# Kernel optimization log

Hardware: AMD Instinct MI355X
Metric: run time of the kernel (lower is better)

## Reference

```python
import jax, jax.numpy as jnp
import numpy as np

N = 50000
E = 800000
IN_C = 256
HID = 256
OUT_C = 64
HEADS = 4
NEG_SLOPE = 0.2  # PyG GATConv default leaky_relu slope


def gat_conv(x, edge_index, W, a_src, a_dst, bias, heads, concat):
    """PyG-style GATConv (add_self_loops=True, eval mode so no dropout).
    x: [N, F_in]; W: [F_in, heads*C]; a_src/a_dst: [heads, C]; bias: [heads*C] or [C].
    """
    n = x.shape[0]
    # add self loops
    loops = jnp.arange(n, dtype=edge_index.dtype)
    src = jnp.concatenate([edge_index[0], loops])
    dst = jnp.concatenate([edge_index[1], loops])
    h = (x @ W).reshape(n, heads, -1)               # [N, H, C]
    alpha_src = jnp.einsum('nhc,hc->nh', h, a_src)  # [N, H]
    alpha_dst = jnp.einsum('nhc,hc->nh', h, a_dst)
    e = jax.nn.leaky_relu(alpha_src[src] + alpha_dst[dst], NEG_SLOPE)  # [E', H]
    # segment softmax over incoming edges of each dst node
    m = jax.ops.segment_max(e, dst, num_segments=n)        # [N, H]
    w = jnp.exp(e - m[dst])
    denom = jax.ops.segment_sum(w, dst, num_segments=n)    # [N, H]
    att = w / (denom[dst] + 1e-16)                          # [E', H]
    out = jax.ops.segment_sum(h[src] * att[:, :, None], dst, num_segments=n)  # [N, H, C]
    out = out.reshape(n, -1) if concat else out.mean(axis=1)
    return out + bias


def setup_inputs() -> dict:
    key = jax.random.key(0)
    ks = jax.random.split(key, 10)
    c1 = HID // HEADS  # per-head channels of layer 1
    s_in = 1.0 / np.sqrt(IN_C)
    s_hid = 1.0 / np.sqrt(HID)
    return {
        'x': jax.random.normal(ks[0], (N, IN_C), dtype=jnp.float32),
        'edge_index': jax.random.randint(ks[1], (2, E), 0, N, dtype=jnp.int64),
        'W1': jax.random.normal(ks[2], (IN_C, HEADS * c1), dtype=jnp.float32) * s_in,
        'a_src1': jax.random.normal(ks[3], (HEADS, c1), dtype=jnp.float32) * s_in,
        'a_dst1': jax.random.normal(ks[4], (HEADS, c1), dtype=jnp.float32) * s_in,
        'b1': jnp.zeros((HEADS * c1,), dtype=jnp.float32),
        'W2': jax.random.normal(ks[5], (HID, OUT_C), dtype=jnp.float32) * s_hid,
        'a_src2': jax.random.normal(ks[6], (1, OUT_C), dtype=jnp.float32) * s_hid,
        'a_dst2': jax.random.normal(ks[7], (1, OUT_C), dtype=jnp.float32) * s_hid,
        'b2': jnp.zeros((OUT_C,), dtype=jnp.float32),
    }


def reference(x, edge_index, W1, a_src1, a_dst1, b1, W2, a_src2, a_dst2, b2):
    h = gat_conv(x, edge_index, W1, a_src1, a_dst1, b1, heads=HEADS, concat=True)
    h = jax.nn.elu(h)
    # dropout: eval mode -> identity
    return gat_conv(h, edge_index, W2, a_src2, a_dst2, b2, heads=1, concat=False)
```

## Files before the change

kernel.cpp:

```cpp
#include <hip/hip_runtime.h>
#include <math.h>

#define NN 50000
#define NE 800000
#define ET (NE + NN)
#define FIN 256
#define HIDC 256
#define OC 64
#define NH 4
#define NEG 0.2f
#define CAP 64
#define NSTRIPES (NN / 16)
#define NGROUPS ((NSTRIPES + 1) / 2)

typedef __attribute__((ext_vector_type(8))) short bf16x8;
typedef __attribute__((ext_vector_type(4))) float f32x4;

__device__ __forceinline__ unsigned short f2bf(float f) {
    unsigned u = __float_as_uint(f);
    unsigned r = (u + 0x7FFFu + ((u >> 16) & 1u)) >> 16;
    return (unsigned short)r;
}
__device__ __forceinline__ float bflo(unsigned v) { return __uint_as_float(v << 16); }
__device__ __forceinline__ float bfhi(unsigned v) { return __uint_as_float(v & 0xffff0000u); }

#define SCB 8
#define NB_SC ((ET + 256 * SCB - 1) / (256 * SCB))
#define NB_CV (NN * FIN / 8 / 256)
#define NB_P1 32
#define NB_P2 8

__device__ __forceinline__ void pack_body(const float* __restrict__ W,
                                          unsigned short* __restrict__ Bp,
                                          int N, int NTL, int t) {
    int lane = t & 63;
    int ntl = (t >> 6) % NTL;
    int ks = ((t >> 6) / NTL) & 7;
    int hy = t / (64 * NTL * 8);
    int col = hy * NTL * 16 + ntl * 16 + (lane & 15);
    int k0 = ks * 32 + (lane >> 4) * 8;
#pragma unroll
    for (int i = 0; i < 8; i++) Bp[(size_t)t * 8 + i] = f2bf(W[(k0 + i) * N + col]);
}

__global__ void k_prep(const int* __restrict__ ei, int* __restrict__ cnt,
                       unsigned short* __restrict__ esrc,
                       const float* __restrict__ x, unsigned short* __restrict__ xb,
                       const float* __restrict__ W1, unsigned short* __restrict__ Bp1,
                       const float* __restrict__ W2, unsigned short* __restrict__ Bp2) {
    int b = blockIdx.x, tid = threadIdx.x;
    if (b < NB_SC) {
        int ebase = b * (256 * SCB) + tid;
        int s[SCB], d[SCB], k[SCB];
        bool v[SCB];
#pragma unroll
        for (int i = 0; i < SCB; i++) {
            int e = ebase + i * 256;
            v[i] = (e < ET);
            s[i] = 0; d[i] = 0;
            if (v[i]) {
                if (e < NE) { s[i] = ei[e]; d[i] = ei[NE + e]; }
                else { s[i] = d[i] = e - NE; }
            }
        }
#pragma unroll
        for (int i = 0; i < SCB; i++)
            if (v[i]) k[i] = atomicAdd(&cnt[d[i]], 1);
#pragma unroll
        for (int i = 0; i < SCB; i++)
            if (v[i] && k[i] < CAP) esrc[(size_t)d[i] * CAP + k[i]] = (unsigned short)s[i];
    } else if (b < NB_SC + NB_CV) {
        int i = ((b - NB_SC) * 256 + tid) * 8;
        float4 f0 = *(const float4*)&x[i];
        float4 f1 = *(const float4*)&x[i + 4];
        uint4 o;
        o.x = (unsigned)f2bf(f0.x) | ((unsigned)f2bf(f0.y) << 16);
        o.y = (unsigned)f2bf(f0.z) | ((unsigned)f2bf(f0.w) << 16);
        o.z = (unsigned)f2bf(f1.x) | ((unsigned)f2bf(f1.y) << 16);
        o.w = (unsigned)f2bf(f1.z) | ((unsigned)f2bf(f1.w) << 16);
        *(uint4*)&xb[i] = o;
    } else if (b < NB_SC + NB_CV + NB_P1) {
        pack_body(W1, Bp1, HIDC, 8, (b - NB_SC - NB_CV) * 256 + tid);
    } else {
        pack_body(W2, Bp2, OC, 4, (b - NB_SC - NB_CV - NB_P1) * 256 + tid);
    }
}

template <int NTL, int NHEADS>
__global__ void __launch_bounds__(256) k_gemm(const unsigned short* __restrict__ A,
                                              const unsigned short* __restrict__ Bp,
                                              unsigned short* __restrict__ D, int N,
                                              const float* __restrict__ aS,
                                              const float* __restrict__ aD,
                                              float* __restrict__ asOut,
                                              float* __restrict__ adOut) {
    constexpr int TOT = 8 * NTL * 64 * 8;
    constexpr int HPH = (NTL * 16) / 64;
    const unsigned short* bsrc = Bp + (size_t)blockIdx.y * TOT;
    int wave = threadIdx.x >> 6, lane = threadIdx.x & 63;
    int l15 = lane & 15, lh = lane >> 4;
    int coloff = blockIdx.y * NTL * 16;
    float aSv[NTL], aDv[NTL];
#pragma unroll
    for (int nt = 0; nt < NTL; nt++) {
        aSv[nt] = aS[coloff + nt * 16 + l15];
        aDv[nt] = aD[coloff + nt * 16 + l15];
    }
    for (int g = blockIdx.x * 4 + wave; g < NGROUPS; g += gridDim.x * 4) {
        int st0 = g * 2;
        bool two = (st0 + 1 < NSTRIPES);
        const unsigned short* arow0 = A + (size_t)(st0 * 16 + l15) * 256 + lh * 8;
        const unsigned short* arow1 = two ? arow0 + 16 * 256 : arow0;
        bf16x8 a0[8], a1[8];
#pragma unroll
        for (int ks = 0; ks < 8; ks++) a0[ks] = *(const bf16x8*)(arow0 + ks * 32);
#pragma unroll
        for (int ks = 0; ks < 8; ks++) a1[ks] = *(const bf16x8*)(arow1 + ks * 32);
        f32x4 acc[2][NTL];
#pragma unroll
        for (int m = 0; m < 2; m++)
#pragma unroll
            for (int t = 0; t < NTL; t++) acc[m][t] = (f32x4){0.f, 0.f, 0.f, 0.f};
#pragma unroll
        for (int ks = 0; ks < 8; ks++) {
#pragma unroll
            for (int nt = 0; nt < NTL; nt++) {
                bf16x8 b = *(const bf16x8*)&bsrc[((size_t)(ks * NTL + nt) * 64 + lane) * 8];
                acc[0][nt] = __builtin_amdgcn_mfma_f32_16x16x32_bf16(a0[ks], b, acc[0][nt], 0, 0, 0);
                acc[1][nt] = __builtin_amdgcn_mfma_f32_16x16x32_bf16(a1[ks], b, acc[1][nt], 0, 0, 0);
            }
        }
        int nm = two ? 2 : 1;
        for (int m = 0; m < nm; m++) {
            int strow = (st0 + m) * 16;
            unsigned short* dbase = D + (size_t)strow * N + coloff;
#pragma unroll
            for (int nt = 0; nt < NTL; nt++)
#pragma unroll
                for (int r = 0; r < 4; r++)
                    dbase[(lh * 4 + r) * N + nt * 16 + l15] = f2bf(acc[m][nt][r]);
#pragma unroll
            for (int r = 0; r < 4; r++) {
#pragma unroll
                for (int gg = 0; gg < HPH; gg++) {
                    float ps = 0.f, pd = 0.f;
#pragma unroll
                    for (int q = 0; q < 4; q++) {
                        int nt = gg * 4 + q;
                        ps += acc[m][nt][r] * aSv[nt];
                        pd += acc[m][nt][r] * aDv[nt];
                    }
#pragma unroll
                    for (int off = 1; off < 16; off <<= 1) {
                        ps += __shfl_xor(ps, off);
                        pd += __shfl_xor(pd, off);
                    }
                    if (l15 == 0) {
                        int row = strow + lh * 4 + r;
                        int hidx = blockIdx.y * HPH + gg;
                        asOut[row * NHEADS + hidx] = ps;
                        adOut[row * NHEADS + hidx] = pd;
                    }
                }
            }
        }
    }
}

__global__ void k_agg1f(const int* __restrict__ cnt, const unsigned short* __restrict__ esrc,
                        const unsigned short* __restrict__ h, const float* __restrict__ as,
                        const float* __restrict__ ad, const float* __restrict__ bias,
                        unsigned short* __restrict__ out) {
    __shared__ float wlds[4][64][4];
    int wave = threadIdx.x >> 6;
    int n = blockIdx.x * 4 + wave;
    int lane = threadIdx.x & 63;
    if (n >= NN) return;
    int deg = cnt[n];
    deg = deg < CAP ? deg : CAP;
    const unsigned short* bucket = &esrc[(size_t)n * CAP];
    bool act = lane < deg;
    int myS = act ? (int)bucket[lane] : 0;
    float4 adv = *(const float4*)&ad[n * NH];
    float e0 = -INFINITY, e1 = -INFINITY, e2 = -INFINITY, e3 = -INFINITY;
    if (act) {
        float4 av = *(const float4*)&as[myS * NH];
        e0 = av.x + adv.x; e0 = e0 > 0.f ? e0 : NEG * e0;
        e1 = av.y + adv.y; e1 = e1 > 0.f ? e1 : NEG * e1;
        e2 = av.z + adv.z; e2 = e2 > 0.f ? e2 : NEG * e2;
        e3 = av.w + adv.w; e3 = e3 > 0.f ? e3 : NEG * e3;
    }
    float m0 = e0, m1 = e1, m2 = e2, m3 = e3;
    for (int off = 32; off; off >>= 1) {
        m0 = fmaxf(m0, __shfl_xor(m0, off));
        m1 = fmaxf(m1, __shfl_xor(m1, off));
        m2 = fmaxf(m2, __shfl_xor(m2, off));
        m3 = fmaxf(m3, __shfl_xor(m3, off));
    }
    float w0 = act ? expf(e0 - m0) : 0.f;
    float w1 = act ? expf(e1 - m1) : 0.f;
    float w2 = act ? expf(e2 - m2) : 0.f;
    float w3 = act ? expf(e3 - m3) : 0.f;
    *(float4*)&wlds[wave][lane][0] = (float4){w0, w1, w2, w3};
    float s0 = w0, s1 = w1, s2 = w2, s3 = w3;
    for (int off = 32; off; off >>= 1) {
        s0 += __shfl_xor(s0, off);
        s1 += __shfl_xor(s1, off);
        s2 += __shfl_xor(s2, off);
        s3 += __shfl_xor(s3, off);
    }
    int hh = lane >> 4;
    int cbase = hh * 64 + (lane & 15) * 4;
    float ssel = hh == 0 ? s0 : hh == 1 ? s1 : hh == 2 ? s2 : s3;
    float rsel = 1.f / (ssel + 1e-16f);
    const float* wcol = &wlds[wave][0][hh];
    const unsigned short* hb = h + cbase;
    float acc0 = 0.f, acc1 = 0.f, acc2 = 0.f, acc3 = 0.f;
    int degP = (deg + 7) & ~7;
    for (int j = 0; j < degP; j += 8) {
        uint2 pv[8];
        float wj[8];
#pragma unroll
        for (int u = 0; u < 8; u++) {
            int s = __shfl(myS, j + u);
            wj[u] = wcol[(j + u) * 4];
            pv[u] = *(const uint2*)&hb[(size_t)s * HIDC];
        }
#pragma unroll
        for (int u = 0; u < 8; u++) {
            acc0 += wj[u] * bflo(pv[u].x);
            acc1 += wj[u] * bfhi(pv[u].x);
            acc2 += wj[u] * bflo(pv[u].y);
            acc3 += wj[u] * bfhi(pv[u].y);
        }
    }
    float4 bv = *(const float4*)&bias[cbase];
    float v0 = acc0 * rsel + bv.x; v0 = v0 > 0.f ? v0 : expm1f(v0);
    float v1 = acc1 * rsel + bv.y; v1 = v1 > 0.f ? v1 : expm1f(v1);
    float v2 = acc2 * rsel + bv.z; v2 = v2 > 0.f ? v2 : expm1f(v2);
    float v3 = acc3 * rsel + bv.w; v3 = v3 > 0.f ? v3 : expm1f(v3);
    uint2 ov;
    ov.x = (unsigned)f2bf(v0) | ((unsigned)f2bf(v1) << 16);
    ov.y = (unsigned)f2bf(v2) | ((unsigned)f2bf(v3) << 16);
    *(uint2*)&out[(size_t)n * HIDC + cbase] = ov;
}

__global__ void k_agg2f(const int* __restrict__ cnt, const unsigned short* __restrict__ esrc,
                        const unsigned short* __restrict__ h, const float* __restrict__ as,
                        const float* __restrict__ ad, const float* __restrict__ bias,
                        float* __restrict__ out) {
    __shared__ float wlds[4][64];
    int wave = threadIdx.x >> 6;
    int n = blockIdx.x * 4 + wave;
    int lane = threadIdx.x & 63;
    if (n >= NN) return;
    int deg = cnt[n];
    deg = deg < CAP ? deg : CAP;
    const unsigned short* bucket = &esrc[(size_t)n * CAP];
    bool act = lane < deg;
    int myS = act ? (int)bucket[lane] : 0;
    float adv = ad[n];
    float e = -INFINITY;
    if (act) {
        e = as[myS] + adv;
        e = e > 0.f ? e : NEG * e;
    }
    float m = e;
    for (int off = 32; off; off >>= 1) m = fmaxf(m, __shfl_xor(m, off));
    float w = act ? expf(e - m) : 0.f;
    wlds[wave][lane] = w;
    float s = w;
    for (int off = 32; off; off >>= 1) s += __shfl_xor(s, off);
    float rd = 1.f / (s + 1e-16f);

    int sub = lane >> 4;
    int cw = (lane & 15) * 4;
    const unsigned short* hb = h + cw;
    float acc0 = 0.f, acc1 = 0.f, acc2 = 0.f, acc3 = 0.f;
    int degP = (deg + 7) & ~7;
    for (int j = 0; j < degP; j += 8) {
        uint2 pv[2];
        float wj[2];
#pragma unroll
        for (int u = 0; u < 2; u++) {
            int jj = j + u * 4 + sub;
            int sj = __shfl(myS, jj);
            wj[u] = wlds[wave][jj];
            pv[u] = *(const uint2*)&hb[(size_t)sj * OC];
        }
#pragma unroll
        for (int u = 0; u < 2; u++) {
            acc0 += wj[u] * bflo(pv[u].x);
            acc1 += wj[u] * bfhi(pv[u].x);
            acc2 += wj[u] * bflo(pv[u].y);
            acc3 += wj[u] * bfhi(pv[u].y);
        }
    }
#pragma unroll
    for (int off = 16; off < 64; off <<= 1) {
        acc0 += __shfl_xor(acc0, off);
        acc1 += __shfl_xor(acc1, off);
        acc2 += __shfl_xor(acc2, off);
        acc3 += __shfl_xor(acc3, off);
    }
    if (lane < 16) {
        float4 bv = *(const float4*)&bias[cw];
        float4 o;
        o.x = acc0 * rd + bv.x;
        o.y = acc1 * rd + bv.y;
        o.z = acc2 * rd + bv.z;
        o.w = acc3 * rd + bv.w;
        *(float4*)&out[(size_t)n * OC + cw] = o;
    }
}

extern "C" void kernel_launch(void* const* d_in, const int* in_sizes, int n_in,
                              void* d_out, int out_size, void* d_ws, size_t ws_size,
                              hipStream_t stream) {
    const float* x   = (const float*)d_in[0];
    const int*   ei  = (const int*)d_in[1];
    const float* W1  = (const float*)d_in[2];
    const float* aS1 = (const float*)d_in[3];
    const float* aD1 = (const float*)d_in[4];
    const float* b1  = (const float*)d_in[5];
    const float* W2  = (const float*)d_in[6];
    const float* aS2 = (const float*)d_in[7];
    const float* aD2 = (const float*)d_in[8];
    const float* b2  = (const float*)d_in[9];
    float* out = (float*)d_out;

    char* p = (char*)d_ws;
    auto alloc = [&](size_t nbytes) {
        char* r = p;
        p += (nbytes + 255) & ~(size_t)255;
        return r;
    };
    unsigned short* xb    = (unsigned short*)alloc((size_t)NN * FIN * 2);
    unsigned short* h1b   = (unsigned short*)alloc((size_t)NN * HIDC * 2);
    unsigned short* act1b = (unsigned short*)alloc((size_t)NN * HIDC * 2);
    unsigned short* h2b   = (unsigned short*)alloc((size_t)NN * OC * 2);
    unsigned short* Bp1   = (unsigned short*)alloc((size_t)2 * 8 * 8 * 64 * 8 * 2);
    unsigned short* Bp2   = (unsigned short*)alloc((size_t)1 * 8 * 4 * 64 * 8 * 2);
    float* as1  = (float*)alloc((size_t)NN * NH * 4);
    float* ad1  = (float*)alloc((size_t)NN * NH * 4);
    float* as2  = (float*)alloc((size_t)NN * 4);
    float* ad2  = (float*)alloc((size_t)NN * 4);
    int*   cnt  = (int*)alloc((size_t)NN * 4);
    unsigned short* esrc = (unsigned short*)alloc((size_t)NN * CAP * 2);

    hipMemsetAsync(cnt, 0, (size_t)NN * 4, stream);

    k_prep<<<NB_SC + NB_CV + NB_P1 + NB_P2, 256, 0, stream>>>(ei, cnt, esrc, x, xb,
                                                              W1, Bp1, W2, Bp2);

    k_gemm<8, NH><<<dim3(391, 2), 256, 0, stream>>>(xb, Bp1, h1b, HIDC, aS1, aD1, as1, ad1);
    k_agg1f<<<(NN + 3) / 4, 256, 0, stream>>>(cnt, esrc, h1b, as1, ad1, b1, act1b);

    k_gemm<4, 1><<<dim3(391, 1), 256, 0, stream>>>(act1b, Bp2, h2b, OC, aS2, aD2, as2, ad2);
    k_agg2f<<<(NN + 3) / 4, 256, 0, stream>>>(cnt, esrc, h2b, as2, ad2, b2, out);
}
```

Before: 203.1 us.

## Move edge scatter from prep kernel into first GEMM launch as extra block row

The CSR-style edge bucketing (atomic counts and source writes) moves out of the prep kernel into a third blockIdx.y slice of the layer-1 GEMM launch. The atomic-heavy scatter can then run alongside the compute-bound GEMM, and the prep kernel shrinks to conversion and weight packing. The GEMM grid x dimension changes to the scatter block count, so GEMM work distribution shifts slightly. The scatter blocks also compete with GEMM blocks for CU slots.

Result: no change. 201.2 us (-0.9%).

```diff
diff --git a/kernel.cpp b/kernel.cpp
--- a/kernel.cpp
+++ b/kernel.cpp
@@ -26,6 +26,32 @@
 
 #define SCB 8
 #define NB_SC ((ET + 256 * SCB - 1) / (256 * SCB))
+
+__device__ __forceinline__ void scatter_body(const int* __restrict__ ei,
+                                             int* __restrict__ cnt,
+                                             unsigned short* __restrict__ esrc,
+                                             int b, int tid) {
+    int ebase = b * (256 * SCB) + tid;
+    int s[SCB], d[SCB], k[SCB];
+    bool v[SCB];
+#pragma unroll
+    for (int i = 0; i < SCB; i++) {
+        int e = ebase + i * 256;
+        v[i] = (e < ET);
+        s[i] = 0; d[i] = 0;
+        if (v[i]) {
+            if (e < NE) { s[i] = ei[e]; d[i] = ei[NE + e]; }
+            else { s[i] = d[i] = e - NE; }
+        }
+    }
+#pragma unroll
+    for (int i = 0; i < SCB; i++)
+        if (v[i]) k[i] = atomicAdd(&cnt[d[i]], 1);
+#pragma unroll
+    for (int i = 0; i < SCB; i++)
+        if (v[i] && k[i] < CAP) esrc[(size_t)d[i] * CAP + k[i]] = (unsigned short)s[i];
+}
+
 #define NB_CV (NN * FIN / 8 / 256)
 #define NB_P1 32
 #define NB_P2 8
@@ -43,34 +69,12 @@
     for (int i = 0; i < 8; i++) Bp[(size_t)t * 8 + i] = f2bf(W[(k0 + i) * N + col]);
 }
 
-__global__ void k_prep(const int* __restrict__ ei, int* __restrict__ cnt,
-                       unsigned short* __restrict__ esrc,
-                       const float* __restrict__ x, unsigned short* __restrict__ xb,
+__global__ void k_prep(const float* __restrict__ x, unsigned short* __restrict__ xb,
                        const float* __restrict__ W1, unsigned short* __restrict__ Bp1,
                        const float* __restrict__ W2, unsigned short* __restrict__ Bp2) {
     int b = blockIdx.x, tid = threadIdx.x;
-    if (b < NB_SC) {
-        int ebase = b * (256 * SCB) + tid;
-        int s[SCB], d[SCB], k[SCB];
-        bool v[SCB];
-#pragma unroll
-        for (int i = 0; i < SCB; i++) {
-            int e = ebase + i * 256;
-            v[i] = (e < ET);
-            s[i] = 0; d[i] = 0;
-            if (v[i]) {
-                if (e < NE) { s[i] = ei[e]; d[i] = ei[NE + e]; }
-                else { s[i] = d[i] = e - NE; }
-            }
-        }
-#pragma unroll
-        for (int i = 0; i < SCB; i++)
-            if (v[i]) k[i] = atomicAdd(&cnt[d[i]], 1);
-#pragma unroll
-        for (int i = 0; i < SCB; i++)
-            if (v[i] && k[i] < CAP) esrc[(size_t)d[i] * CAP + k[i]] = (unsigned short)s[i];
-    } else if (b < NB_SC + NB_CV) {
-        int i = ((b - NB_SC) * 256 + tid) * 8;
+    if (b < NB_CV) {
+        int i = (b * 256 + tid) * 8;
         float4 f0 = *(const float4*)&x[i];
         float4 f1 = *(const float4*)&x[i + 4];
         uint4 o;
@@ -79,23 +83,30 @@
         o.z = (unsigned)f2bf(f1.x) | ((unsigned)f2bf(f1.y) << 16);
         o.w = (unsigned)f2bf(f1.z) | ((unsigned)f2bf(f1.w) << 16);
         *(uint4*)&xb[i] = o;
-    } else if (b < NB_SC + NB_CV + NB_P1) {
-        pack_body(W1, Bp1, HIDC, 8, (b - NB_SC - NB_CV) * 256 + tid);
+    } else if (b < NB_CV + NB_P1) {
+        pack_body(W1, Bp1, HIDC, 8, (b - NB_CV) * 256 + tid);
     } else {
-        pack_body(W2, Bp2, OC, 4, (b - NB_SC - NB_CV - NB_P1) * 256 + tid);
-    }
-}
-
-template <int NTL, int NHEADS>
+        pack_body(W2, Bp2, OC, 4, (b - NB_CV - NB_P1) * 256 + tid);
+    }
+}
+
+template <int NTL, int NHEADS, bool SCAT>
 __global__ void __launch_bounds__(256) k_gemm(const unsigned short* __restrict__ A,
                                               const unsigned short* __restrict__ Bp,
                                               unsigned short* __restrict__ D, int N,
                                               const float* __restrict__ aS,
                                               const float* __restrict__ aD,
                                               float* __restrict__ asOut,
-                                              float* __restrict__ adOut) {
+                                              float* __restrict__ adOut,
+                                              const int* __restrict__ ei,
+                                              int* __restrict__ cnt,
+                                              unsigned short* __restrict__ esrc) {
     constexpr int TOT = 8 * NTL * 64 * 8;
     constexpr int HPH = (NTL * 16) / 64;
+    if (SCAT && blockIdx.y == 2) {
+        scatter_body(ei, cnt, esrc, blockIdx.x, threadIdx.x);
+        return;
+    }
     const unsigned short* bsrc = Bp + (size_t)blockIdx.y * TOT;
     int wave = threadIdx.x >> 6, lane = threadIdx.x & 63;
     int l15 = lane & 15, lh = lane >> 4;
@@ -350,12 +361,15 @@
 
     hipMemsetAsync(cnt, 0, (size_t)NN * 4, stream);
 
-    k_prep<<<NB_SC + NB_CV + NB_P1 + NB_P2, 256, 0, stream>>>(ei, cnt, esrc, x, xb,
-                                                              W1, Bp1, W2, Bp2);
-
-    k_gemm<8, NH><<<dim3(391, 2), 256, 0, stream>>>(xb, Bp1, h1b, HIDC, aS1, aD1, as1, ad1);
+    k_prep<<<NB_CV + NB_P1 + NB_P2, 256, 0, stream>>>(x, xb, W1, Bp1, W2, Bp2);
+
+    k_gemm<8, NH, true><<<dim3(NB_SC, 3), 256, 0, stream>>>(xb, Bp1, h1b, HIDC,
+                                                            aS1, aD1, as1, ad1,
+                                                            ei, cnt, esrc);
     k_agg1f<<<(NN + 3) / 4, 256, 0, stream>>>(cnt, esrc, h1b, as1, ad1, b1, act1b);
 
-    k_gemm<4, 1><<<dim3(391, 1), 256, 0, stream>>>(act1b, Bp2, h2b, OC, aS2, aD2, as2, ad2);
+    k_gemm<4, 1, false><<<dim3(391, 1), 256, 0, stream>>>(act1b, Bp2, h2b, OC,
+                                                          aS2, aD2, as2, ad2,
+                                                          nullptr, nullptr, nullptr);
     k_agg2f<<<(NN + 3) / 4, 256, 0, stream>>>(cnt, esrc, h2b, as2, ad2, b2, out);
 }
```
